# Kernel tuning notes

Measured on AMD Instinct MI355X. Metric: run time of the kernel, lower is better.

## Reference

```python
import jax, jax.numpy as jnp
import numpy as np
from jax import lax

SCOPE = 15
RICKER_WIDTH = 3.0
DAMP = 0.12
MAX_STEPS = 10


def mexican_hat(scope, width, damping):
    # ricker / mexican-hat wavelet sampled at `scope` integer-spaced points, scaled by damping
    x = np.linspace(-(scope // 2), scope // 2, scope).astype(np.float32)
    norm = 2.0 / (np.sqrt(3.0 * width) * np.pi ** 0.25)
    w = damping * norm * (1.0 - (x / width) ** 2) * np.exp(-(x ** 2) / (2.0 * width ** 2))
    return jnp.asarray(w, dtype=jnp.float32)


def setup_inputs() -> dict:
    key = jax.random.key(0)
    activations = jax.random.normal(key, (32, 256, 56, 56), dtype=jnp.float32)
    w_rec = mexican_hat(SCOPE, RICKER_WIDTH, DAMP)  # [scope]
    return {"activations": activations, "w_rec": w_rec, "max_steps": MAX_STEPS}


def reference(activations, w_rec, max_steps):
    # activations: [B, C, H, W]; inhibition conv runs along the C axis only.
    scope = w_rec.shape[0]
    pad = scope // 2
    x = activations[:, None]                     # [B, 1, C, H, W]
    kernel = w_rec.reshape(1, 1, scope, 1, 1)    # OIDHW

    def conv(y):
        return lax.conv_general_dilated(
            y, kernel,
            window_strides=(1, 1, 1),
            padding=[(pad, pad), (0, 0), (0, 0)],
            dimension_numbers=("NCDHW", "OIDHW", "NCDHW"),
        )

    # fixed-point iteration: state <- activations + W_rec * state  (threshold=0 => always max_steps iters)
    state = x
    for _ in range(max_steps):
        state = x + conv(state)
    return state[:, 0]  # squeeze channel dim -> [B, C, H, W]
```

## Files before the change

kernel.cpp:

```cpp
#include <hip/hip_runtime.h>


#define NCH 256
#define PAD 7
#define SCOPE 15
#define SPATIAL 3136
#define PER_B 802816
#define STW 32
#define STILES_PER_B 98
#define NTILES 3136
#define MAXCH 12

typedef __attribute__((ext_vector_type(8))) __bf16 bf16x8;
typedef __attribute__((ext_vector_type(16))) float float16;
typedef __attribute__((ext_vector_type(4))) unsigned int uint4v;
typedef __attribute__((ext_vector_type(2))) unsigned int uint2v;

static __device__ __forceinline__ unsigned short f2bf_rn_u(float f) {
  unsigned u = __builtin_bit_cast(unsigned int, f);
  return (unsigned short)((u + 0x7FFFu + ((u >> 16) & 1u)) >> 16);
}
static __device__ __forceinline__ float bf2f_u(unsigned short h) {
  unsigned u = ((unsigned)h) << 16;
  return __builtin_bit_cast(float, u);
}
static __device__ __forceinline__ unsigned pack_bf2(float a, float b) {
  return (unsigned)f2bf_rn_u(a) | ((unsigned)f2bf_rn_u(b) << 16);
}
static __device__ __forceinline__ void split2(float a, float b,
                                              unsigned& h, unsigned& l) {
  h = pack_bf2(a, b);
  const float ra = a - __builtin_bit_cast(float, h << 16);
  const float rb = b - __builtin_bit_cast(float, h & 0xFFFF0000u);
  l = pack_bf2(ra, rb);
}

__global__ void build_M_kernel(const float* __restrict__ w,
                               const int* __restrict__ max_steps_p,
                               unsigned short* __restrict__ AhF,
                               unsigned short* __restrict__ AlF) {
  const int d = blockIdx.x;
  const int c = threadIdx.x;
  __shared__ float v[2][NCH];
  __shared__ float wsh[SCOPE];
  if (c < SCOPE) wsh[c] = w[c];
  const float e = (c == d) ? 1.0f : 0.0f;
  v[0][c] = e;
  __syncthreads();
  const int steps = *max_steps_p;
  int cur = 0;
  for (int t = 0; t < steps; ++t) {
    float s = e;
#pragma unroll
    for (int j = 0; j < SCOPE; ++j) {
      const int cc = c + j - PAD;
      if (cc >= 0 && cc < NCH) s += wsh[j] * v[cur][cc];
    }
    cur ^= 1;
    v[cur][c] = s;
    __syncthreads();
  }
  const float f = v[cur][c];
  const unsigned short h = f2bf_rn_u(f);
  const unsigned short l = f2bf_rn_u(f - bf2f_u(h));

  const int wv = c >> 5;
  const int c0 = wv * 32;
  int clo = c0 - 70; if (clo < 0) clo = 0; clo >>= 4;
  int chi = c0 + 101; if (chi > 255) chi = 255; chi >>= 4;
  const int ch = d >> 4;
  if (ch >= clo && ch <= chi) {
    const int i    = ch - clo;
    const int half = (d >> 3) & 1;
    const int j    = d & 7;
    const int lane = half * 32 + (c & 31);
    const size_t dst = ((size_t)(wv * MAXCH + i) * 64 + lane) * 8 + j;
    AhF[dst] = h;
    AlF[dst] = l;
  }
}

__global__ __launch_bounds__(512, 8) void apply_M_kernel(
    const float* __restrict__ x, const unsigned short* __restrict__ AhF,
    const unsigned short* __restrict__ AlF, float* __restrict__ out) {
  __shared__ unsigned XB[8192];

  const int tid  = threadIdx.x;
  const int lane = tid & 63;
  const int w    = tid >> 6;
  const int m    = lane & 31;
  const int half = lane >> 5;
  const int c0   = w * 32;

  int clo = c0 - 70; if (clo < 0) clo = 0; clo >>= 4;
  int chi = c0 + 101; if (chi > 255) chi = 255; chi >>= 4;
  const int nch = chi - clo + 1;

  const int sq = (tid & 7) * 4;
  const int dg = tid >> 3;

  const int tau = blockIdx.x;
  const float* gb = x + (size_t)(tau / STILES_PER_B) * PER_B
                      + (size_t)(tau % STILES_PER_B) * STW;
  const float4 g0 = *(const float4*)(gb + (size_t)(2 * dg) * SPATIAL + sq);
  const float4 g1 = *(const float4*)(gb + (size_t)(2 * dg + 1) * SPATIAL + sq);
  const float4 g2 = *(const float4*)(gb + (size_t)(2 * dg + 128) * SPATIAL + sq);
  const float4 g3 = *(const float4*)(gb + (size_t)(2 * dg + 129) * SPATIAL + sq);

  {
    unsigned h0, h1, h2, h3, l0, l1, l2, l3;
    split2(g0.x, g1.x, h0, l0); split2(g0.y, g1.y, h1, l1);
    split2(g0.z, g1.z, h2, l2); split2(g0.w, g1.w, h3, l3);
    unsigned* p = &XB[dg * 64 + sq * 2];
    *(uint4v*)(p)     = (uint4v){h0, l0, h1, l1};
    *(uint4v*)(p + 4) = (uint4v){h2, l2, h3, l3};
    split2(g2.x, g3.x, h0, l0); split2(g2.y, g3.y, h1, l1);
    split2(g2.z, g3.z, h2, l2); split2(g2.w, g3.w, h3, l3);
    unsigned* q = &XB[(dg + 64) * 64 + sq * 2];
    *(uint4v*)(q)     = (uint4v){h0, l0, h1, l1};
    *(uint4v*)(q + 4) = (uint4v){h2, l2, h3, l3};
  }
  __syncthreads();

  const unsigned short* mhp = AhF + ((size_t)(w * MAXCH) * 64 + lane) * 8;
  const unsigned short* mlp = AlF + ((size_t)(w * MAXCH) * 64 + lane) * 8;
  asm volatile("" : "+v"(mhp), "+v"(mlp));

  float16 a0, a1;
#pragma unroll
  for (int q = 0; q < 16; ++q) { a0[q] = 0.0f; a1[q] = 0.0f; }

#pragma unroll
  for (int i = 0; i < MAXCH; ++i) {
    if (i < nch) {
      const bf16x8 Ah = *(const bf16x8*)(mhp + i * 512);
      const bf16x8 Al = *(const bf16x8*)(mlp + i * 512);
      const int k2b = (clo + i) * 8 + half * 4;
      const unsigned* bp = &XB[k2b * 64 + 2 * m];
      const uint2v r0 = *(const uint2v*)(bp);
      const uint2v r1 = *(const uint2v*)(bp + 64);
      const uint2v r2 = *(const uint2v*)(bp + 128);
      const uint2v r3 = *(const uint2v*)(bp + 192);
      const uint4v hw = {r0.x, r1.x, r2.x, r3.x};
      const uint4v lw = {r0.y, r1.y, r2.y, r3.y};
      const bf16x8 bh = __builtin_bit_cast(bf16x8, hw);
      const bf16x8 bl = __builtin_bit_cast(bf16x8, lw);
      a0 = __builtin_amdgcn_mfma_f32_32x32x16_bf16(Ah, bh, a0, 0, 0, 0);
      a1 = __builtin_amdgcn_mfma_f32_32x32x16_bf16(Ah, bl, a1, 0, 0, 0);
      a1 = __builtin_amdgcn_mfma_f32_32x32x16_bf16(Al, bh, a1, 0, 0, 0);
    }
  }

  const int b  = tau / STILES_PER_B;
  const int s0 = (tau % STILES_PER_B) * STW;
  float* ob = out + (size_t)b * PER_B + (size_t)s0 + m;
#pragma unroll
  for (int r = 0; r < 16; ++r) {
    const int row = (r & 3) + 8 * (r >> 2) + 4 * half;
    ob[(size_t)(c0 + row) * SPATIAL] = a0[r] + a1[r];
  }
}

extern "C" void kernel_launch(void* const* d_in, const int* in_sizes, int n_in,
                              void* d_out, int out_size, void* d_ws, size_t ws_size,
                              hipStream_t stream) {
  const float* x = (const float*)d_in[0];
  const float* w = (const float*)d_in[1];
  const int* ms = (const int*)d_in[2];
  float* out = (float*)d_out;

  unsigned short* AhF = (unsigned short*)d_ws;
  unsigned short* AlF = AhF + 8 * MAXCH * 64 * 8;

  build_M_kernel<<<NCH, NCH, 0, stream>>>(w, ms, AhF, AlF);
  apply_M_kernel<<<NTILES, 512, 0, stream>>>(x, AhF, AlF, out);
}
```

Before: 208.4 us.

## Software-pipeline M-matrix loads in groups of three and use single accumulator

Restructures the MFMA loop into a double-buffered, three-chunk-per-stage pipeline. The first M fragments are issued before the x split and the LDS barrier, and later groups are prefetched while the current group computes. The two accumulators are merged into one, which makes the three MFMAs per chunk a dependent chain, and occupancy is lowered from 8 to 6 waves in the launch bounds to make room for the prefetch registers. The syncthreads is replaced by an explicit lgkmcnt wait plus s_barrier. The longer MFMA dependency chain and lower occupancy could offset the latency hiding.

```diff
diff --git a/kernel.cpp b/kernel.cpp
--- a/kernel.cpp
+++ b/kernel.cpp
@@ -80,7 +80,35 @@
   }
 }
 
-__global__ __launch_bounds__(512, 8) void apply_M_kernel(
+
+#define LOADA(dh, dl, i)                                   \
+  {                                                        \
+    dh = *(const bf16x8*)(mhp + (i) * 512);                \
+    dl = *(const bf16x8*)(mlp + (i) * 512);                \
+  }
+#define LOADA_P(dh, dl, i)                                 \
+  if ((i) < nch) LOADA(dh, dl, i)
+
+#define CHUNK(Ahr, Alr, i)                                              \
+  {                                                                     \
+    const int k2b = (clo + (i)) * 8 + half * 4;                         \
+    const unsigned* bp = &XB[k2b * 64 + 2 * m];                         \
+    const uint2v r0 = *(const uint2v*)(bp);                             \
+    const uint2v r1 = *(const uint2v*)(bp + 64);                        \
+    const uint2v r2 = *(const uint2v*)(bp + 128);                       \
+    const uint2v r3 = *(const uint2v*)(bp + 192);                       \
+    const uint4v hw = {r0.x, r1.x, r2.x, r3.x};                         \
+    const uint4v lw = {r0.y, r1.y, r2.y, r3.y};                         \
+    const bf16x8 bh = __builtin_bit_cast(bf16x8, hw);                   \
+    const bf16x8 bl = __builtin_bit_cast(bf16x8, lw);                   \
+    acc = __builtin_amdgcn_mfma_f32_32x32x16_bf16(Ahr, bh, acc, 0, 0, 0); \
+    acc = __builtin_amdgcn_mfma_f32_32x32x16_bf16(Ahr, bl, acc, 0, 0, 0); \
+    acc = __builtin_amdgcn_mfma_f32_32x32x16_bf16(Alr, bh, acc, 0, 0, 0); \
+  }
+#define CHUNK_P(Ahr, Alr, i)                               \
+  if ((i) < nch) CHUNK(Ahr, Alr, i)
+
+__global__ __launch_bounds__(512, 6) void apply_M_kernel(
     const float* __restrict__ x, const unsigned short* __restrict__ AhF,
     const unsigned short* __restrict__ AlF, float* __restrict__ out) {
   __shared__ unsigned XB[8192];
@@ -106,6 +134,13 @@
   const float4 g1 = *(const float4*)(gb + (size_t)(2 * dg + 1) * SPATIAL + sq);
   const float4 g2 = *(const float4*)(gb + (size_t)(2 * dg + 128) * SPATIAL + sq);
   const float4 g3 = *(const float4*)(gb + (size_t)(2 * dg + 129) * SPATIAL + sq);
+
+  const unsigned short* mhp = AhF + ((size_t)(w * MAXCH) * 64 + lane) * 8;
+  const unsigned short* mlp = AlF + ((size_t)(w * MAXCH) * 64 + lane) * 8;
+
+  bf16x8 pH0, pL0, pH1, pL1, pH2, pL2;
+  bf16x8 qH0, qL0, qH1, qL1, qH2, qL2;
+  LOADA(pH0, pL0, 0) LOADA(pH1, pL1, 1) LOADA(pH2, pL2, 2)
 
   {
     unsigned h0, h1, h2, h3, l0, l1, l2, l3;
@@ -120,36 +155,24 @@
     *(uint4v*)(q)     = (uint4v){h0, l0, h1, l1};
     *(uint4v*)(q + 4) = (uint4v){h2, l2, h3, l3};
   }
-  __syncthreads();
-
-  const unsigned short* mhp = AhF + ((size_t)(w * MAXCH) * 64 + lane) * 8;
-  const unsigned short* mlp = AlF + ((size_t)(w * MAXCH) * 64 + lane) * 8;
-  asm volatile("" : "+v"(mhp), "+v"(mlp));
-
-  float16 a0, a1;
+
+  asm volatile("s_waitcnt lgkmcnt(0)" ::: "memory");
+  __builtin_amdgcn_s_barrier();
+
+  float16 acc;
 #pragma unroll
-  for (int q = 0; q < 16; ++q) { a0[q] = 0.0f; a1[q] = 0.0f; }
-
-#pragma unroll
-  for (int i = 0; i < MAXCH; ++i) {
-    if (i < nch) {
-      const bf16x8 Ah = *(const bf16x8*)(mhp + i * 512);
-      const bf16x8 Al = *(const bf16x8*)(mlp + i * 512);
-      const int k2b = (clo + i) * 8 + half * 4;
-      const unsigned* bp = &XB[k2b * 64 + 2 * m];
-      const uint2v r0 = *(const uint2v*)(bp);
-      const uint2v r1 = *(const uint2v*)(bp + 64);
-      const uint2v r2 = *(const uint2v*)(bp + 128);
-      const uint2v r3 = *(const uint2v*)(bp + 192);
-      const uint4v hw = {r0.x, r1.x, r2.x, r3.x};
-      const uint4v lw = {r0.y, r1.y, r2.y, r3.y};
-      const bf16x8 bh = __builtin_bit_cast(bf16x8, hw);
-      const bf16x8 bl = __builtin_bit_cast(bf16x8, lw);
-      a0 = __builtin_amdgcn_mfma_f32_32x32x16_bf16(Ah, bh, a0, 0, 0, 0);
-      a1 = __builtin_amdgcn_mfma_f32_32x32x16_bf16(Ah, bl, a1, 0, 0, 0);
-      a1 = __builtin_amdgcn_mfma_f32_32x32x16_bf16(Al, bh, a1, 0, 0, 0);
-    }
-  }
+  for (int q = 0; q < 16; ++q) acc[q] = 0.0f;
+
+  LOADA(qH0, qL0, 3) LOADA(qH1, qL1, 4) LOADA(qH2, qL2, 5)
+  CHUNK(pH0, pL0, 0) CHUNK(pH1, pL1, 1) CHUNK(pH2, pL2, 2)
+
+  LOADA(pH0, pL0, 6) LOADA_P(pH1, pL1, 7) LOADA_P(pH2, pL2, 8)
+  CHUNK(qH0, qL0, 3) CHUNK(qH1, qL1, 4) CHUNK(qH2, qL2, 5)
+
+  LOADA_P(qH0, qL0, 9) LOADA_P(qH1, qL1, 10) LOADA_P(qH2, qL2, 11)
+  CHUNK(pH0, pL0, 6) CHUNK_P(pH1, pL1, 7) CHUNK_P(pH2, pL2, 8)
+
+  CHUNK_P(qH0, qL0, 9) CHUNK_P(qH1, qL1, 10) CHUNK_P(qH2, qL2, 11)
 
   const int b  = tau / STILES_PER_B;
   const int s0 = (tau % STILES_PER_B) * STW;
@@ -157,7 +180,7 @@
 #pragma unroll
   for (int r = 0; r < 16; ++r) {
     const int row = (r & 3) + 8 * (r >> 2) + 4 * half;
-    ob[(size_t)(c0 + row) * SPATIAL] = a0[r] + a1[r];
+    ob[(size_t)(c0 + row) * SPATIAL] = acc[r];
   }
 }
 
```

New measurement: 230.4 us. 1.11x slower.
